# Kernel tuning notes

Measured on AMD Instinct MI355X. Metric: run time of the kernel, lower is better.

The kernel has to match this reference:

```python
import jax, jax.numpy as jnp
import numpy as np

N_NODES = 100000
N_EDGES = 600000
D_IN = 128
D_HID = 128


def gcn_conv(x, W, b, src, dst, n_nodes):
    # PyG GCNConv: add self-loops, symmetric deg^-1/2 normalization,
    # linear transform, scatter-add aggregation, bias.
    xw = x @ W  # [N, H]
    self_loop = jnp.arange(n_nodes, dtype=src.dtype)
    s = jnp.concatenate([src, self_loop])  # sources j
    d = jnp.concatenate([dst, self_loop])  # targets i
    deg = jax.ops.segment_sum(jnp.ones_like(d, dtype=xw.dtype), d,
                              num_segments=n_nodes)
    dinv = jnp.where(deg > 0, jax.lax.rsqrt(deg), 0.0)
    norm = dinv[s] * dinv[d]  # [E+N]
    msg = xw[s] * norm[:, None]  # gather + scale
    out = jax.ops.segment_sum(msg, d, num_segments=n_nodes)
    return out + b


def setup_inputs() -> dict:
    key = jax.random.key(0)
    ks = jax.random.split(key, 4)
    x = jax.random.normal(ks[0], (N_NODES, D_IN), dtype=jnp.float32)
    edge_index = jax.random.randint(ks[1], (2, N_EDGES), 0, N_NODES,
                                    dtype=jnp.int32)
    W1 = jax.random.normal(ks[2], (D_IN, D_HID), dtype=jnp.float32) / np.sqrt(D_IN)
    b1 = jnp.zeros((D_HID,), dtype=jnp.float32)
    W2 = jax.random.normal(ks[3], (D_HID, D_HID), dtype=jnp.float32) / np.sqrt(D_HID)
    b2 = jnp.zeros((D_HID,), dtype=jnp.float32)
    return {"x": x, "edge_index": edge_index, "W1": W1, "b1": b1,
            "W2": W2, "b2": b2}


def reference(x, edge_index, W1, b1, W2, b2):
    src, dst = edge_index[0], edge_index[1]
    n = x.shape[0]
    z = gcn_conv(x, W1, b1, src, dst, n)
    z = jax.nn.relu(z)
    z = gcn_conv(z, W2, b2, src, dst, n)
    # decode: per-edge dot product of endpoint embeddings
    return jnp.sum(z[src] * z[dst], axis=1)  # [E]
```

## Files before the change

kernel.cpp:

```cpp
#include <hip/hip_runtime.h>


typedef __attribute__((ext_vector_type(8))) short short8;
typedef __attribute__((ext_vector_type(4))) float f32x4;

__device__ __forceinline__ unsigned bf16_rne(float x) {
  unsigned u = __builtin_bit_cast(unsigned, x);
  return (u + 0x7FFFu + ((u >> 16) & 1u)) >> 16;
}
__device__ __forceinline__ float bf2f(unsigned short u) {
  return __builtin_bit_cast(float, ((unsigned)u) << 16);
}

__global__ __launch_bounds__(256) void deg_kernel(const int* __restrict__ dst,
                                                  int* __restrict__ deg, int E) {
  int e = blockIdx.x * 256 + threadIdx.x;
  if (e < E) atomicAdd(&deg[dst[e]], 1);
}

__global__ __launch_bounds__(512) void scan1_kernel(const int* __restrict__ in,
                                                    int* __restrict__ tmp,
                                                    int* __restrict__ bsums, int n) {
  __shared__ int sm[2][512];
  int t = threadIdx.x;
  int gid = blockIdx.x * 512 + t;
  int v = (gid < n) ? in[gid] : 0;
  int pp = 0;
  sm[0][t] = v;
  __syncthreads();
  for (int off = 1; off < 512; off <<= 1) {
    int nv = sm[pp][t];
    if (t >= off) nv += sm[pp][t - off];
    sm[pp ^ 1][t] = nv;
    pp ^= 1;
    __syncthreads();
  }
  int inc = sm[pp][t];
  if (gid < n) tmp[gid] = inc;
  if (t == 511) bsums[blockIdx.x] = inc;
}

__global__ __launch_bounds__(256) void scan2_kernel(int* bsums, int nb) {
  __shared__ int sm[2][256];
  int t = threadIdx.x;
  int v = (t < nb) ? bsums[t] : 0;
  int pp = 0;
  sm[0][t] = v;
  __syncthreads();
  for (int off = 1; off < 256; off <<= 1) {
    int nv = sm[pp][t];
    if (t >= off) nv += sm[pp][t - off];
    sm[pp ^ 1][t] = nv;
    pp ^= 1;
    __syncthreads();
  }
  int inc = sm[pp][t];
  if (t < nb) bsums[t] = inc - v;
}

__global__ __launch_bounds__(256) void scan3_kernel(const int* __restrict__ tmp,
                                                    const int* __restrict__ bsums,
                                                    const int* __restrict__ deg,
                                                    int* __restrict__ rowptr,
                                                    float* __restrict__ dinv, int n) {
  int gid = blockIdx.x * 256 + threadIdx.x;
  if (gid < n) {
    rowptr[gid + 1] = tmp[gid] + bsums[gid >> 9];
    dinv[gid] = rsqrtf((float)(deg[gid] + 1));
  }
  if (gid == 0) rowptr[0] = 0;
}

__global__ __launch_bounds__(256) void scatter_kernel(const int* __restrict__ src,
                                                      const int* __restrict__ dst,
                                                      const int* __restrict__ rowptr,
                                                      int* __restrict__ cnt,
                                                      int* __restrict__ csr_src,
                                                      int* __restrict__ csr_eid, int E) {
  int e = blockIdx.x * 256 + threadIdx.x;
  if (e < E) {
    int d = dst[e];
    int pos = rowptr[d] + atomicAdd(&cnt[d], 1);
    csr_src[pos] = src[e];
    csr_eid[pos] = e;
  }
}

__global__ __launch_bounds__(256) void xbf_kernel(const float* __restrict__ x,
                                                  unsigned short* __restrict__ xb,
                                                  int total8) {
  int i = blockIdx.x * 256 + threadIdx.x;
  if (i >= total8) return;
  const float4* p = (const float4*)x + (size_t)i * 2;
  float4 a = p[0], b = p[1];
  float av[8] = {a.x, a.y, a.z, a.w, b.x, b.y, b.z, b.w};
  short8 o;
#pragma unroll
  for (int j = 0; j < 8; ++j) o[j] = (short)bf16_rne(av[j]);
  ((short8*)xb)[i] = o;
}

__global__ __launch_bounds__(256) void wpack_kernel(const float* __restrict__ W,
                                                    short* __restrict__ Wp) {
  int t = blockIdx.x * 256 + threadIdx.x;
  if (t >= 2048) return;
  int lane = t & 63;
  int kf = (t >> 6) & 3;
  int ct = t >> 8;
  int col = ct * 16 + (lane & 15);
  int k0 = kf * 32 + (lane >> 4) * 8;
  short* dh = Wp + ((((0 * 8 + ct) * 4 + kf) * 64) + lane) * 8;
  short* dl = Wp + ((((1 * 8 + ct) * 4 + kf) * 64) + lane) * 8;
  for (int j = 0; j < 8; ++j) {
    float w = W[(k0 + j) * 128 + col];
    unsigned h = bf16_rne(w);
    float hf = __builtin_bit_cast(float, h << 16);
    unsigned lo = bf16_rne(w - hf);
    dh[j] = (short)h;
    dl[j] = (short)lo;
  }
}

__global__ __launch_bounds__(256) void gemm_kernel(const unsigned short* __restrict__ A,
                                                   const short* __restrict__ Wp,
                                                   const float* __restrict__ dinv,
                                                   unsigned short* __restrict__ out,
                                                   int M) {
  const int wave = threadIdx.x >> 6;
  const int lane = threadIdx.x & 63;
  const int quad = lane >> 4;
  const int l15 = lane & 15;

  short8 Bh[2][4], Bl[2][4];
  const short8* Wp8 = (const short8*)Wp;
#pragma unroll
  for (int c = 0; c < 2; ++c) {
    int ct = wave * 2 + c;
#pragma unroll
    for (int f = 0; f < 4; ++f) {
      Bh[c][f] = Wp8[((0 * 8 + ct) * 4 + f) * 64 + lane];
      Bl[c][f] = Wp8[((1 * 8 + ct) * 4 + f) * 64 + lane];
    }
  }

  int rb0 = blockIdx.x * 64;
  const int colbase = wave * 32 + l15;
#pragma unroll 1
  for (int s = 0; s < 4; ++s) {
    int rb = rb0 + s * 16;
    if (rb >= M) break;
    int arow = rb + l15;
    bool rok = arow < M;
    short8 af[4];
#pragma unroll
    for (int f = 0; f < 4; ++f) {
      if (rok) {
        af[f] = *(const short8*)(A + (size_t)arow * 128 + f * 32 + quad * 8);
      } else {
        short8 z = {0, 0, 0, 0, 0, 0, 0, 0};
        af[f] = z;
      }
    }
    f32x4 acc0 = {0.f, 0.f, 0.f, 0.f};
    f32x4 acc1 = {0.f, 0.f, 0.f, 0.f};
#pragma unroll
    for (int f = 0; f < 4; ++f) {
      acc0 = __builtin_amdgcn_mfma_f32_16x16x32_bf16(af[f], Bh[0][f], acc0, 0, 0, 0);
      acc1 = __builtin_amdgcn_mfma_f32_16x16x32_bf16(af[f], Bh[1][f], acc1, 0, 0, 0);
      acc0 = __builtin_amdgcn_mfma_f32_16x16x32_bf16(af[f], Bl[0][f], acc0, 0, 0, 0);
      acc1 = __builtin_amdgcn_mfma_f32_16x16x32_bf16(af[f], Bl[1][f], acc1, 0, 0, 0);
    }
#pragma unroll
    for (int i = 0; i < 4; ++i) {
      int r = rb + quad * 4 + i;
      if (r < M) {
        float d = dinv[r];
        out[(size_t)r * 128 + colbase] = (unsigned short)bf16_rne(acc0[i] * d);
        out[(size_t)r * 128 + colbase + 16] = (unsigned short)bf16_rne(acc1[i] * d);
      }
    }
  }
}

__global__ __launch_bounds__(256) void agg_kernel(const unsigned short* __restrict__ xw,
                                                  const float* __restrict__ dinv,
                                                  const int* __restrict__ rowptr,
                                                  const int* __restrict__ csr,
                                                  const float* __restrict__ bias,
                                                  unsigned short* __restrict__ out,
                                                  int relu, int N) {
  int node = blockIdx.x * 16 + (threadIdx.x >> 4);
  int l = threadIdx.x & 15;
  if (node >= N) return;
  const short8* xw8 = (const short8*)xw;
  short8 sv = xw8[(size_t)node * 16 + l];
  float acc[8];
#pragma unroll
  for (int j = 0; j < 8; ++j) acc[j] = bf2f((unsigned short)sv[j]);
  int s = rowptr[node], e = rowptr[node + 1];
  int k = s;
  for (; k + 4 <= e; k += 4) {
    int j0 = csr[k], j1 = csr[k + 1], j2 = csr[k + 2], j3 = csr[k + 3];
    short8 v0 = xw8[(size_t)j0 * 16 + l];
    short8 v1 = xw8[(size_t)j1 * 16 + l];
    short8 v2 = xw8[(size_t)j2 * 16 + l];
    short8 v3 = xw8[(size_t)j3 * 16 + l];
#pragma unroll
    for (int j = 0; j < 8; ++j) {
      acc[j] += (bf2f((unsigned short)v0[j]) + bf2f((unsigned short)v1[j])) +
                (bf2f((unsigned short)v2[j]) + bf2f((unsigned short)v3[j]));
    }
  }
  for (; k < e; ++k) {
    short8 v = xw8[(size_t)csr[k] * 16 + l];
#pragma unroll
    for (int j = 0; j < 8; ++j) acc[j] += bf2f((unsigned short)v[j]);
  }
  float di = dinv[node];
  const float4* b4 = (const float4*)bias;
  float4 bb0 = b4[l * 2], bb1 = b4[l * 2 + 1];
  float bv[8] = {bb0.x, bb0.y, bb0.z, bb0.w, bb1.x, bb1.y, bb1.z, bb1.w};
  short8 o;
#pragma unroll
  for (int j = 0; j < 8; ++j) {
    float v = fmaf(di, acc[j], bv[j]);
    if (relu) v = fmaxf(v, 0.f);
    o[j] = (short)bf16_rne(v);
  }
  ((short8*)out)[(size_t)node * 16 + l] = o;
}

__global__ __launch_bounds__(256) void decode_kernel(const unsigned short* __restrict__ z,
                                                     const int* __restrict__ rowptr,
                                                     const int* __restrict__ csr_src,
                                                     const int* __restrict__ csr_eid,
                                                     float* __restrict__ out, int N) {
  int node = blockIdx.x * 16 + (threadIdx.x >> 4);
  int l = threadIdx.x & 15;
  if (node >= N) return;
  const short8* z8 = (const short8*)z;
  short8 zv = z8[(size_t)node * 16 + l];
  float zd[8];
#pragma unroll
  for (int j = 0; j < 8; ++j) zd[j] = bf2f((unsigned short)zv[j]);
  int s = rowptr[node], e = rowptr[node + 1];
  int k = s;
  for (; k + 4 <= e; k += 4) {
    int j0 = csr_src[k], j1 = csr_src[k + 1];
    int j2 = csr_src[k + 2], j3 = csr_src[k + 3];
    short8 v0 = z8[(size_t)j0 * 16 + l];
    short8 v1 = z8[(size_t)j1 * 16 + l];
    short8 v2 = z8[(size_t)j2 * 16 + l];
    short8 v3 = z8[(size_t)j3 * 16 + l];
    float p0 = 0.f, p1 = 0.f, p2 = 0.f, p3 = 0.f;
#pragma unroll
    for (int j = 0; j < 8; ++j) {
      p0 = fmaf(zd[j], bf2f((unsigned short)v0[j]), p0);
      p1 = fmaf(zd[j], bf2f((unsigned short)v1[j]), p1);
      p2 = fmaf(zd[j], bf2f((unsigned short)v2[j]), p2);
      p3 = fmaf(zd[j], bf2f((unsigned short)v3[j]), p3);
    }
#pragma unroll
    for (int off = 8; off > 0; off >>= 1) {
      p0 += __shfl_xor(p0, off);
      p1 += __shfl_xor(p1, off);
      p2 += __shfl_xor(p2, off);
      p3 += __shfl_xor(p3, off);
    }
    if (l == 0) {
      out[csr_eid[k]] = p0;
      out[csr_eid[k + 1]] = p1;
      out[csr_eid[k + 2]] = p2;
      out[csr_eid[k + 3]] = p3;
    }
  }
  for (; k < e; ++k) {
    short8 v = z8[(size_t)csr_src[k] * 16 + l];
    float p = 0.f;
#pragma unroll
    for (int j = 0; j < 8; ++j) p = fmaf(zd[j], bf2f((unsigned short)v[j]), p);
#pragma unroll
    for (int off = 8; off > 0; off >>= 1) p += __shfl_xor(p, off);
    if (l == 0) out[csr_eid[k]] = p;
  }
}

extern "C" void kernel_launch(void* const* d_in, const int* in_sizes, int n_in,
                              void* d_out, int out_size, void* d_ws, size_t ws_size,
                              hipStream_t stream) {
  const float* x  = (const float*)d_in[0];
  const int*   ei = (const int*)d_in[1];
  const float* W1 = (const float*)d_in[2];
  const float* b1 = (const float*)d_in[3];
  const float* W2 = (const float*)d_in[4];
  const float* b2 = (const float*)d_in[5];

  const int N = in_sizes[0] / 128;
  const int E = in_sizes[1] / 2;
  const int* src = ei;
  const int* dst = ei + E;

  char* ws = (char*)d_ws;
  size_t off = 0;
  auto alloc = [&](size_t bytes) -> void* {
    void* p = ws + off;
    off += (bytes + 255) & ~(size_t)255;
    return p;
  };
  unsigned short* xb   = (unsigned short*)alloc((size_t)N * 128 * 2);
  unsigned short* bufA = (unsigned short*)alloc((size_t)N * 128 * 2);
  unsigned short* bufB = (unsigned short*)alloc((size_t)N * 128 * 2);
  float* dinv    = (float*)alloc((size_t)N * 4);
  int*   rowptr  = (int*)alloc((size_t)(N + 1) * 4);
  int*   csr_src = (int*)alloc((size_t)E * 4);
  int*   csr_eid = (int*)alloc((size_t)E * 4);
  short* Wp1     = (short*)alloc((size_t)2 * 8 * 4 * 64 * 8 * 2);
  short* Wp2     = (short*)alloc((size_t)2 * 8 * 4 * 64 * 8 * 2);
  int*   tmp     = (int*)alloc((size_t)N * 4);
  int*   deg     = (int*)alloc((size_t)N * 4);
  int*   cnt     = (int*)alloc((size_t)N * 4);
  int*   bsums   = (int*)alloc(1024);
  size_t zbytes = ((char*)bsums + 1024) - (char*)deg;
  hipMemsetAsync(deg, 0, zbytes, stream);

  const int EB = (E + 255) / 256;
  const int NB = (N + 255) / 256;
  const int SB = (N + 511) / 512;
  const int total8 = N * 16;

  xbf_kernel<<<(total8 + 255) / 256, 256, 0, stream>>>(x, xb, total8);
  wpack_kernel<<<8, 256, 0, stream>>>(W1, Wp1);
  wpack_kernel<<<8, 256, 0, stream>>>(W2, Wp2);

  deg_kernel<<<EB, 256, 0, stream>>>(dst, deg, E);
  scan1_kernel<<<SB, 512, 0, stream>>>(deg, tmp, bsums, N);
  scan2_kernel<<<1, 256, 0, stream>>>(bsums, SB);
  scan3_kernel<<<NB, 256, 0, stream>>>(tmp, bsums, deg, rowptr, dinv, N);
  scatter_kernel<<<EB, 256, 0, stream>>>(src, dst, rowptr, cnt, csr_src, csr_eid, E);

  const int GB = (N + 63) / 64;
  const int AB = (N + 15) / 16;
  const int DB = (N + 15) / 16;

  gemm_kernel<<<GB, 256, 0, stream>>>(xb, Wp1, dinv, bufA, N);
  agg_kernel<<<AB, 256, 0, stream>>>(bufA, dinv, rowptr, csr_src, b1, bufB, 1, N);
  gemm_kernel<<<GB, 256, 0, stream>>>(bufB, Wp2, dinv, bufA, N);
  agg_kernel<<<AB, 256, 0, stream>>>(bufA, dinv, rowptr, csr_src, b2, bufB, 0, N);
  decode_kernel<<<DB, 256, 0, stream>>>(bufB, rowptr, csr_src, csr_eid,
                                        (float*)d_out, N);
}
```

Baseline: 323.0 us.

## Fuse input bf16 conversion into first GEMM and interleave CSR src/eid arrays

Drops the standalone x-to-bf16 kernel and converts fp32 rows to bf16 inside the first GEMM's A-tile load. This removes one full write and read of a 25 MB intermediate. The separate csr_src and csr_eid arrays become one int2 array, so decode fetches both fields with one load. The degree and scatter kernels now handle four edges per thread. The agg kernels read the wider int2 entries but use only the source index, which wastes some bandwidth there.

```diff
diff --git a/kernel.cpp b/kernel.cpp
--- a/kernel.cpp
+++ b/kernel.cpp
@@ -14,8 +14,12 @@
 
 __global__ __launch_bounds__(256) void deg_kernel(const int* __restrict__ dst,
                                                   int* __restrict__ deg, int E) {
-  int e = blockIdx.x * 256 + threadIdx.x;
-  if (e < E) atomicAdd(&deg[dst[e]], 1);
+  int base = blockIdx.x * 1024 + threadIdx.x;
+#pragma unroll
+  for (int i = 0; i < 4; ++i) {
+    int e = base + i * 256;
+    if (e < E) atomicAdd(&deg[dst[e]], 1);
+  }
 }
 
 __global__ __launch_bounds__(512) void scan1_kernel(const int* __restrict__ in,
@@ -75,29 +79,17 @@
                                                       const int* __restrict__ dst,
                                                       const int* __restrict__ rowptr,
                                                       int* __restrict__ cnt,
-                                                      int* __restrict__ csr_src,
-                                                      int* __restrict__ csr_eid, int E) {
-  int e = blockIdx.x * 256 + threadIdx.x;
-  if (e < E) {
-    int d = dst[e];
-    int pos = rowptr[d] + atomicAdd(&cnt[d], 1);
-    csr_src[pos] = src[e];
-    csr_eid[pos] = e;
-  }
-}
-
-__global__ __launch_bounds__(256) void xbf_kernel(const float* __restrict__ x,
-                                                  unsigned short* __restrict__ xb,
-                                                  int total8) {
-  int i = blockIdx.x * 256 + threadIdx.x;
-  if (i >= total8) return;
-  const float4* p = (const float4*)x + (size_t)i * 2;
-  float4 a = p[0], b = p[1];
-  float av[8] = {a.x, a.y, a.z, a.w, b.x, b.y, b.z, b.w};
-  short8 o;
-#pragma unroll
-  for (int j = 0; j < 8; ++j) o[j] = (short)bf16_rne(av[j]);
-  ((short8*)xb)[i] = o;
+                                                      int2* __restrict__ csr, int E) {
+  int base = blockIdx.x * 1024 + threadIdx.x;
+#pragma unroll
+  for (int i = 0; i < 4; ++i) {
+    int e = base + i * 256;
+    if (e < E) {
+      int d = dst[e];
+      int pos = rowptr[d] + atomicAdd(&cnt[d], 1);
+      csr[pos] = make_int2(src[e], e);
+    }
+  }
 }
 
 __global__ __launch_bounds__(256) void wpack_kernel(const float* __restrict__ W,
@@ -121,7 +113,8 @@
   }
 }
 
-__global__ __launch_bounds__(256) void gemm_kernel(const unsigned short* __restrict__ A,
+template <bool FP32A>
+__global__ __launch_bounds__(256) void gemm_kernel(const void* __restrict__ Av,
                                                    const short* __restrict__ Wp,
                                                    const float* __restrict__ dinv,
                                                    unsigned short* __restrict__ out,
@@ -155,7 +148,17 @@
 #pragma unroll
     for (int f = 0; f < 4; ++f) {
       if (rok) {
-        af[f] = *(const short8*)(A + (size_t)arow * 128 + f * 32 + quad * 8);
+        if constexpr (FP32A) {
+          const float4* A4 = (const float4*)Av + (size_t)arow * 32;
+          float4 a0 = A4[f * 8 + quad * 2];
+          float4 a1 = A4[f * 8 + quad * 2 + 1];
+          float av[8] = {a0.x, a0.y, a0.z, a0.w, a1.x, a1.y, a1.z, a1.w};
+#pragma unroll
+          for (int j = 0; j < 8; ++j) af[f][j] = (short)bf16_rne(av[j]);
+        } else {
+          af[f] = *(const short8*)((const unsigned short*)Av +
+                                   (size_t)arow * 128 + f * 32 + quad * 8);
+        }
       } else {
         short8 z = {0, 0, 0, 0, 0, 0, 0, 0};
         af[f] = z;
@@ -185,7 +188,7 @@
 __global__ __launch_bounds__(256) void agg_kernel(const unsigned short* __restrict__ xw,
                                                   const float* __restrict__ dinv,
                                                   const int* __restrict__ rowptr,
-                                                  const int* __restrict__ csr,
+                                                  const int2* __restrict__ csr,
                                                   const float* __restrict__ bias,
                                                   unsigned short* __restrict__ out,
                                                   int relu, int N) {
@@ -200,7 +203,7 @@
   int s = rowptr[node], e = rowptr[node + 1];
   int k = s;
   for (; k + 4 <= e; k += 4) {
-    int j0 = csr[k], j1 = csr[k + 1], j2 = csr[k + 2], j3 = csr[k + 3];
+    int j0 = csr[k].x, j1 = csr[k + 1].x, j2 = csr[k + 2].x, j3 = csr[k + 3].x;
     short8 v0 = xw8[(size_t)j0 * 16 + l];
     short8 v1 = xw8[(size_t)j1 * 16 + l];
     short8 v2 = xw8[(size_t)j2 * 16 + l];
@@ -212,7 +215,7 @@
     }
   }
   for (; k < e; ++k) {
-    short8 v = xw8[(size_t)csr[k] * 16 + l];
+    short8 v = xw8[(size_t)csr[k].x * 16 + l];
 #pragma unroll
     for (int j = 0; j < 8; ++j) acc[j] += bf2f((unsigned short)v[j]);
   }
@@ -232,8 +235,7 @@
 
 __global__ __launch_bounds__(256) void decode_kernel(const unsigned short* __restrict__ z,
                                                      const int* __restrict__ rowptr,
-                                                     const int* __restrict__ csr_src,
-                                                     const int* __restrict__ csr_eid,
+                                                     const int2* __restrict__ csr,
                                                      float* __restrict__ out, int N) {
   int node = blockIdx.x * 16 + (threadIdx.x >> 4);
   int l = threadIdx.x & 15;
@@ -246,12 +248,11 @@
   int s = rowptr[node], e = rowptr[node + 1];
   int k = s;
   for (; k + 4 <= e; k += 4) {
-    int j0 = csr_src[k], j1 = csr_src[k + 1];
-    int j2 = csr_src[k + 2], j3 = csr_src[k + 3];
-    short8 v0 = z8[(size_t)j0 * 16 + l];
-    short8 v1 = z8[(size_t)j1 * 16 + l];
-    short8 v2 = z8[(size_t)j2 * 16 + l];
-    short8 v3 = z8[(size_t)j3 * 16 + l];
+    int2 c0 = csr[k], c1 = csr[k + 1], c2 = csr[k + 2], c3 = csr[k + 3];
+    short8 v0 = z8[(size_t)c0.x * 16 + l];
+    short8 v1 = z8[(size_t)c1.x * 16 + l];
+    short8 v2 = z8[(size_t)c2.x * 16 + l];
+    short8 v3 = z8[(size_t)c3.x * 16 + l];
     float p0 = 0.f, p1 = 0.f, p2 = 0.f, p3 = 0.f;
 #pragma unroll
     for (int j = 0; j < 8; ++j) {
@@ -268,20 +269,21 @@
       p3 += __shfl_xor(p3, off);
     }
     if (l == 0) {
-      out[csr_eid[k]] = p0;
-      out[csr_eid[k + 1]] = p1;
-      out[csr_eid[k + 2]] = p2;
-      out[csr_eid[k + 3]] = p3;
+      out[c0.y] = p0;
+      out[c1.y] = p1;
+      out[c2.y] = p2;
+      out[c3.y] = p3;
     }
   }
   for (; k < e; ++k) {
-    short8 v = z8[(size_t)csr_src[k] * 16 + l];
+    int2 c = csr[k];
+    short8 v = z8[(size_t)c.x * 16 + l];
     float p = 0.f;
 #pragma unroll
     for (int j = 0; j < 8; ++j) p = fmaf(zd[j], bf2f((unsigned short)v[j]), p);
 #pragma unroll
     for (int off = 8; off > 0; off >>= 1) p += __shfl_xor(p, off);
-    if (l == 0) out[csr_eid[k]] = p;
+    if (l == 0) out[c.y] = p;
   }
 }
 
@@ -307,13 +309,11 @@
     off += (bytes + 255) & ~(size_t)255;
     return p;
   };
-  unsigned short* xb   = (unsigned short*)alloc((size_t)N * 128 * 2);
   unsigned short* bufA = (unsigned short*)alloc((size_t)N * 128 * 2);
   unsigned short* bufB = (unsigned short*)alloc((size_t)N * 128 * 2);
   float* dinv    = (float*)alloc((size_t)N * 4);
   int*   rowptr  = (int*)alloc((size_t)(N + 1) * 4);
-  int*   csr_src = (int*)alloc((size_t)E * 4);
-  int*   csr_eid = (int*)alloc((size_t)E * 4);
+  int2*  csr     = (int2*)alloc((size_t)E * 8);
   short* Wp1     = (short*)alloc((size_t)2 * 8 * 4 * 64 * 8 * 2);
   short* Wp2     = (short*)alloc((size_t)2 * 8 * 4 * 64 * 8 * 2);
   int*   tmp     = (int*)alloc((size_t)N * 4);
@@ -323,29 +323,26 @@
   size_t zbytes = ((char*)bsums + 1024) - (char*)deg;
   hipMemsetAsync(deg, 0, zbytes, stream);
 
-  const int EB = (E + 255) / 256;
+  const int E4B = (E + 1023) / 1024;
   const int NB = (N + 255) / 256;
   const int SB = (N + 511) / 512;
-  const int total8 = N * 16;
-
-  xbf_kernel<<<(total8 + 255) / 256, 256, 0, stream>>>(x, xb, total8);
+
   wpack_kernel<<<8, 256, 0, stream>>>(W1, Wp1);
   wpack_kernel<<<8, 256, 0, stream>>>(W2, Wp2);
 
-  deg_kernel<<<EB, 256, 0, stream>>>(dst, deg, E);
+  deg_kernel<<<E4B, 256, 0, stream>>>(dst, deg, E);
   scan1_kernel<<<SB, 512, 0, stream>>>(deg, tmp, bsums, N);
   scan2_kernel<<<1, 256, 0, stream>>>(bsums, SB);
   scan3_kernel<<<NB, 256, 0, stream>>>(tmp, bsums, deg, rowptr, dinv, N);
-  scatter_kernel<<<EB, 256, 0, stream>>>(src, dst, rowptr, cnt, csr_src, csr_eid, E);
+  scatter_kernel<<<E4B, 256, 0, stream>>>(src, dst, rowptr, cnt, csr, E);
 
   const int GB = (N + 63) / 64;
   const int AB = (N + 15) / 16;
   const int DB = (N + 15) / 16;
 
-  gemm_kernel<<<GB, 256, 0, stream>>>(xb, Wp1, dinv, bufA, N);
-  agg_kernel<<<AB, 256, 0, stream>>>(bufA, dinv, rowptr, csr_src, b1, bufB, 1, N);
-  gemm_kernel<<<GB, 256, 0, stream>>>(bufB, Wp2, dinv, bufA, N);
-  agg_kernel<<<AB, 256, 0, stream>>>(bufA, dinv, rowptr, csr_src, b2, bufB, 0, N);
-  decode_kernel<<<DB, 256, 0, stream>>>(bufB, rowptr, csr_src, csr_eid,
-                                        (float*)d_out, N);
-}
+  gemm_kernel<true><<<GB, 256, 0, stream>>>(x, Wp1, dinv, bufA, N);
+  agg_kernel<<<AB, 256, 0, stream>>>(bufA, dinv, rowptr, csr, b1, bufB, 1, N);
+  gemm_kernel<false><<<GB, 256, 0, stream>>>(bufB, Wp2, dinv, bufA, N);
+  agg_kernel<<<AB, 256, 0, stream>>>(bufA, dinv, rowptr, csr, b2, bufB, 0, N);
+  decode_kernel<<<DB, 256, 0, stream>>>(bufB, rowptr, csr, (float*)d_out, N);
+}
```

After: 321.7 us. No clear change (-0.4%).
